# Optimization experiments

Measured on AMD Instinct MI355X. Metric: run time of the kernel, lower is better.

## Reference

```python
import jax, jax.numpy as jnp
import numpy as np

GAMMA = 0.99
CLIP_VALUE = 5.0
B, T = 4096, 2048


def setup_inputs() -> dict:
    key = jax.random.key(0)
    k1, k2, k3, k4 = jax.random.split(key, 4)
    return {
        "log_probs": jax.random.normal(k1, (B, T), dtype=jnp.float32),
        "logits": jax.random.normal(k2, (B, T, 1), dtype=jnp.float32),
        "weight": jax.random.uniform(k3, (B, T), dtype=jnp.float32),
        "baselines": jax.random.normal(k4, (B, T, 1), dtype=jnp.float32),
    }


def _discounted_cumulative(wr, gamma):
    # wr: [B, T]. cum[t] = sum_{s>=t} gamma^(s-t) * wr[s]
    # Reverse-time linear recurrence: c[t] = wr[t] + gamma * c[t+1]
    def step(c, x):
        c = x + gamma * c
        return c, c
    # scan over time in reverse; xs laid out time-major [T, B]
    _, cum_rev = jax.lax.scan(step, jnp.zeros(wr.shape[0], wr.dtype), wr[:, ::-1].T)
    return cum_rev[::-1].T  # back to [B, T]


def reference(log_probs, logits, weight, baselines):
    rewards = jax.nn.log_sigmoid(logits[..., 0])          # [B, T]
    cumulative_rewards = _discounted_cumulative(weight * rewards, GAMMA)  # [B, T]
    advantages = cumulative_rewards - baselines[..., 0]
    advantages = advantages - advantages.mean(axis=0)      # center over batch
    advantages = jnp.clip(advantages, -CLIP_VALUE, CLIP_VALUE)
    generator_objective = (advantages * log_probs).sum(axis=0)  # [T]
    return (generator_objective, cumulative_rewards)
```

## Files before the change

### kernel.cpp

```cpp
#include <hip/hip_runtime.h>
#include <math.h>

#define BDIM 4096
#define TDIM 2048
#define NBLK 512
#define RPB  8

constexpr double gpow(int e) {
    double r = 1.0;
    for (int i = 0; i < e; ++i) r *= 0.99;
    return r;
}

__device__ __forceinline__ float logsig_fast(float x) {
    float z = __expf(-fabsf(x));
    return fminf(x, 0.0f) - __logf(1.0f + z);
}

__device__ __forceinline__ float clip5(float x) {
    return fminf(fmaxf(x, -5.0f), 5.0f);
}

__global__ __launch_bounds__(512) void k1_scan(
    const float* __restrict__ logits,
    const float* __restrict__ weight,
    const float* __restrict__ baselines,
    float* __restrict__ cum_out,
    float* __restrict__ partial,
    float* __restrict__ colsum,
    float* __restrict__ obj)
{
    const int tid  = threadIdx.x;
    const int lane = tid & 63;
    const int wave = tid >> 6;
    const int t0   = tid * 4;

    if (blockIdx.x == 0) {
        *reinterpret_cast<float4*>(colsum + t0) = make_float4(0.f, 0.f, 0.f, 0.f);
    }
    if (blockIdx.x == 1) {
        *reinterpret_cast<float4*>(obj + t0) = make_float4(0.f, 0.f, 0.f, 0.f);
    }

    const float G    = 0.99f;
    const float G256 = (float)gpow(256);
    const float LOG2G = -0.014499569695115089f;
    const float gk[4] = {(float)gpow(4), (float)gpow(3), (float)gpow(2), (float)gpow(1)};
    const float fs[6] = {(float)gpow(4),  (float)gpow(8),  (float)gpow(16),
                         (float)gpow(32), (float)gpow(64), (float)gpow(128)};
    const float lane_pow = exp2f((float)((64 - lane) * 4) * LOG2G);

    __shared__ float wsum[2][8];

    float colacc[4];
#pragma unroll
    for (int k = 0; k < 4; ++k) colacc[k] = 0.0f;

    const int row0 = blockIdx.x * RPB;
    size_t base = (size_t)row0 * TDIM + t0;

    float4 x0 = *reinterpret_cast<const float4*>(logits + base);
    float4 w0 = *reinterpret_cast<const float4*>(weight + base);
    float4 b0 = *reinterpret_cast<const float4*>(baselines + base);

    for (int r = 0; r < RPB; ++r) {
        const size_t nbase = base + TDIM;
        const bool has_next = (r + 1 < RPB);

        float wr[4];
        wr[0] = w0.x * logsig_fast(x0.x); wr[1] = w0.y * logsig_fast(x0.y);
        wr[2] = w0.z * logsig_fast(x0.z); wr[3] = w0.w * logsig_fast(x0.w);

        float4 nx0, nw0, nb0;
        if (has_next) {
            nx0 = *reinterpret_cast<const float4*>(logits + nbase);
            nw0 = *reinterpret_cast<const float4*>(weight + nbase);
            nb0 = *reinterpret_cast<const float4*>(baselines + nbase);
        }

        float loc[4];
        loc[3] = wr[3];
#pragma unroll
        for (int k = 2; k >= 0; --k) loc[k] = fmaf(G, loc[k + 1], wr[k]);

        float v = loc[0];
#pragma unroll
        for (int s = 0; s < 6; ++s) {
            const int o = 1 << s;
            float up = __shfl_down(v, (unsigned)o, 64);
            if (lane + o < 64) v = fmaf(fs[s], up, v);
        }

        const int buf = r & 1;
        if (lane == 0) wsum[buf][wave] = v;
        __syncthreads();
        const float W1 = wsum[buf][1], W2 = wsum[buf][2], W3 = wsum[buf][3];
        const float W4 = wsum[buf][4], W5 = wsum[buf][5], W6 = wsum[buf][6];
        const float W7 = wsum[buf][7];
        const float C6 = W7;
        const float C5 = fmaf(G256, C6, W6);
        const float C4 = fmaf(G256, C5, W5);
        const float C3 = fmaf(G256, C4, W4);
        const float C2 = fmaf(G256, C3, W3);
        const float C1 = fmaf(G256, C2, W2);
        const float C0 = fmaf(G256, C1, W1);
        const float carry = (wave == 0) ? C0 : (wave == 1) ? C1 : (wave == 2) ? C2 :
                            (wave == 3) ? C3 : (wave == 4) ? C4 : (wave == 5) ? C5 :
                            (wave == 6) ? C6 : 0.0f;

        const float vfull = fmaf(lane_pow, carry, v);
        const float vn = __shfl_down(vfull, 1, 64);
        const float tail = (lane == 63) ? carry : vn;

        float c[4];
#pragma unroll
        for (int k = 0; k < 4; ++k) c[k] = fmaf(gk[k], tail, loc[k]);

        *reinterpret_cast<float4*>(cum_out + base) = make_float4(c[0], c[1], c[2], c[3]);

        colacc[0] += c[0] - b0.x; colacc[1] += c[1] - b0.y;
        colacc[2] += c[2] - b0.z; colacc[3] += c[3] - b0.w;

        base = nbase;
        if (has_next) {
            x0 = nx0; w0 = nw0; b0 = nb0;
        }
    }

    const size_t pbase = (size_t)blockIdx.x * TDIM + t0;
    *reinterpret_cast<float4*>(partial + pbase) =
        make_float4(colacc[0], colacc[1], colacc[2], colacc[3]);
}

__global__ __launch_bounds__(256) void k2_colsum(
    const float* __restrict__ partial, float* __restrict__ colsum)
{
    const int gid = blockIdx.x * 256 + threadIdx.x;
    const int col = gid & (TDIM - 1);
    const int slc = gid >> 11;
    const float* p = partial + (size_t)slc * 16 * TDIM + col;
    float s = 0.0f;
#pragma unroll
    for (int i = 0; i < 16; ++i) s += p[(size_t)i * TDIM];
    atomicAdd(colsum + col, s);
}

#define K3_ROWS 8
__global__ __launch_bounds__(256) void k3_part(
    const float* __restrict__ cum,
    const float* __restrict__ baselines,
    const float* __restrict__ lp,
    const float* __restrict__ colsum,
    float* __restrict__ objpart)
{
    const int c2 = (blockIdx.x * 256 + threadIdx.x) * 2;
    const int yb = blockIdx.y;
    const int r0 = yb * K3_ROWS;
    const float inv = 1.0f / (float)BDIM;
    float2 ms = *reinterpret_cast<const float2*>(colsum + c2);
    const float m0 = ms.x * inv, m1 = ms.y * inv;

    float a0 = 0.0f, a1 = 0.0f;
    size_t idx = (size_t)r0 * TDIM + c2;
#pragma unroll
    for (int r = 0; r < K3_ROWS; ++r, idx += TDIM) {
        float2 c = *reinterpret_cast<const float2*>(cum + idx);
        float2 b = *reinterpret_cast<const float2*>(baselines + idx);
        float2 l = *reinterpret_cast<const float2*>(lp + idx);
        a0 = fmaf(clip5(c.x - b.x - m0), l.x, a0);
        a1 = fmaf(clip5(c.y - b.y - m1), l.y, a1);
    }
    *reinterpret_cast<float2*>(objpart + (size_t)yb * TDIM + c2) = make_float2(a0, a1);
}

__global__ __launch_bounds__(256) void k4_objsum(
    const float* __restrict__ objpart, float* __restrict__ obj)
{
    const int gid = blockIdx.x * 256 + threadIdx.x;
    const int col = gid & (TDIM - 1);
    const int slc = gid >> 11;
    const float* p = objpart + (size_t)slc * 16 * TDIM + col;
    float s = 0.0f;
#pragma unroll
    for (int i = 0; i < 16; ++i) s += p[(size_t)i * TDIM];
    atomicAdd(obj + col, s);
}

extern "C" void kernel_launch(void* const* d_in, const int* in_sizes, int n_in,
                              void* d_out, int out_size, void* d_ws, size_t ws_size,
                              hipStream_t stream) {
    const float* log_probs = (const float*)d_in[0];
    const float* logits    = (const float*)d_in[1];
    const float* weight    = (const float*)d_in[2];
    const float* baselines = (const float*)d_in[3];

    float* out = (float*)d_out;
    float* obj = out;
    float* cum = out + TDIM;

    float* partial = (float*)d_ws;
    float* colsum  = partial + (size_t)NBLK * TDIM;

    k1_scan<<<NBLK, 512, 0, stream>>>(logits, weight, baselines, cum, partial, colsum, obj);
    k2_colsum<<<256, 256, 0, stream>>>(partial, colsum);
    k3_part<<<dim3(4, 512), 256, 0, stream>>>(cum, baselines, log_probs, colsum, partial);
    k4_objsum<<<256, 256, 0, stream>>>(partial, obj);
}
```

Baseline: 162.0 us.

## Scan each row with 1024 threads of two elements instead of 512 of four

The row-scan kernel now launches 1024 threads per block, each handling two time steps with float2 loads, instead of 512 threads handling four. The intra-wave shuffle scan and the 16-wave cross-wave carry chain are adjusted to the new powers of gamma. The aim is more threads in flight for latency hiding on the memory-bound pass. In exchange, loads are narrower, the serial carry chain across waves is longer, and the per-row block barrier now spans 16 waves.

Measured after the change: 163.1 us. About the same (+0.7%).

```diff
diff --git a/kernel.cpp b/kernel.cpp
--- a/kernel.cpp
+++ b/kernel.cpp
@@ -21,7 +21,7 @@
     return fminf(fmaxf(x, -5.0f), 5.0f);
 }
 
-__global__ __launch_bounds__(512) void k1_scan(
+__global__ __launch_bounds__(1024, 8) void k1_scan(
     const float* __restrict__ logits,
     const float* __restrict__ weight,
     const float* __restrict__ baselines,
@@ -33,55 +33,53 @@
     const int tid  = threadIdx.x;
     const int lane = tid & 63;
     const int wave = tid >> 6;
-    const int t0   = tid * 4;
+    const int t0   = tid * 2;
 
     if (blockIdx.x == 0) {
-        *reinterpret_cast<float4*>(colsum + t0) = make_float4(0.f, 0.f, 0.f, 0.f);
+        *reinterpret_cast<float2*>(colsum + t0) = make_float2(0.f, 0.f);
     }
     if (blockIdx.x == 1) {
-        *reinterpret_cast<float4*>(obj + t0) = make_float4(0.f, 0.f, 0.f, 0.f);
+        *reinterpret_cast<float2*>(obj + t0) = make_float2(0.f, 0.f);
     }
 
     const float G    = 0.99f;
-    const float G256 = (float)gpow(256);
+    const float G128 = (float)gpow(128);
     const float LOG2G = -0.014499569695115089f;
-    const float gk[4] = {(float)gpow(4), (float)gpow(3), (float)gpow(2), (float)gpow(1)};
-    const float fs[6] = {(float)gpow(4),  (float)gpow(8),  (float)gpow(16),
-                         (float)gpow(32), (float)gpow(64), (float)gpow(128)};
-    const float lane_pow = exp2f((float)((64 - lane) * 4) * LOG2G);
-
-    __shared__ float wsum[2][8];
-
-    float colacc[4];
-#pragma unroll
-    for (int k = 0; k < 4; ++k) colacc[k] = 0.0f;
+    const float gk[2] = {(float)gpow(2), (float)gpow(1)};
+    const float fs[6] = {(float)gpow(2),  (float)gpow(4),  (float)gpow(8),
+                         (float)gpow(16), (float)gpow(32), (float)gpow(64)};
+    const float lane_pow = exp2f((float)((64 - lane) * 2) * LOG2G);
+
+    __shared__ float wsum[2][16];
+
+    float colacc[2];
+    colacc[0] = 0.0f; colacc[1] = 0.0f;
 
     const int row0 = blockIdx.x * RPB;
     size_t base = (size_t)row0 * TDIM + t0;
 
-    float4 x0 = *reinterpret_cast<const float4*>(logits + base);
-    float4 w0 = *reinterpret_cast<const float4*>(weight + base);
-    float4 b0 = *reinterpret_cast<const float4*>(baselines + base);
+    float2 x0 = *reinterpret_cast<const float2*>(logits + base);
+    float2 w0 = *reinterpret_cast<const float2*>(weight + base);
+    float2 b0 = *reinterpret_cast<const float2*>(baselines + base);
 
     for (int r = 0; r < RPB; ++r) {
         const size_t nbase = base + TDIM;
         const bool has_next = (r + 1 < RPB);
 
-        float wr[4];
-        wr[0] = w0.x * logsig_fast(x0.x); wr[1] = w0.y * logsig_fast(x0.y);
-        wr[2] = w0.z * logsig_fast(x0.z); wr[3] = w0.w * logsig_fast(x0.w);
-
-        float4 nx0, nw0, nb0;
+        float wr[2];
+        wr[0] = w0.x * logsig_fast(x0.x);
+        wr[1] = w0.y * logsig_fast(x0.y);
+
+        float2 nx0, nw0, nb0;
         if (has_next) {
-            nx0 = *reinterpret_cast<const float4*>(logits + nbase);
-            nw0 = *reinterpret_cast<const float4*>(weight + nbase);
-            nb0 = *reinterpret_cast<const float4*>(baselines + nbase);
+            nx0 = *reinterpret_cast<const float2*>(logits + nbase);
+            nw0 = *reinterpret_cast<const float2*>(weight + nbase);
+            nb0 = *reinterpret_cast<const float2*>(baselines + nbase);
         }
 
-        float loc[4];
-        loc[3] = wr[3];
-#pragma unroll
-        for (int k = 2; k >= 0; --k) loc[k] = fmaf(G, loc[k + 1], wr[k]);
+        float loc[2];
+        loc[1] = wr[1];
+        loc[0] = fmaf(G, wr[1], wr[0]);
 
         float v = loc[0];
 #pragma unroll
@@ -94,32 +92,45 @@
         const int buf = r & 1;
         if (lane == 0) wsum[buf][wave] = v;
         __syncthreads();
-        const float W1 = wsum[buf][1], W2 = wsum[buf][2], W3 = wsum[buf][3];
-        const float W4 = wsum[buf][4], W5 = wsum[buf][5], W6 = wsum[buf][6];
-        const float W7 = wsum[buf][7];
-        const float C6 = W7;
-        const float C5 = fmaf(G256, C6, W6);
-        const float C4 = fmaf(G256, C5, W5);
-        const float C3 = fmaf(G256, C4, W4);
-        const float C2 = fmaf(G256, C3, W3);
-        const float C1 = fmaf(G256, C2, W2);
-        const float C0 = fmaf(G256, C1, W1);
-        const float carry = (wave == 0) ? C0 : (wave == 1) ? C1 : (wave == 2) ? C2 :
-                            (wave == 3) ? C3 : (wave == 4) ? C4 : (wave == 5) ? C5 :
-                            (wave == 6) ? C6 : 0.0f;
+        const float W1  = wsum[buf][1],  W2  = wsum[buf][2],  W3  = wsum[buf][3];
+        const float W4  = wsum[buf][4],  W5  = wsum[buf][5],  W6  = wsum[buf][6];
+        const float W7  = wsum[buf][7],  W8  = wsum[buf][8],  W9  = wsum[buf][9];
+        const float W10 = wsum[buf][10], W11 = wsum[buf][11], W12 = wsum[buf][12];
+        const float W13 = wsum[buf][13], W14 = wsum[buf][14], W15 = wsum[buf][15];
+        const float C14 = W15;
+        const float C13 = fmaf(G128, C14, W14);
+        const float C12 = fmaf(G128, C13, W13);
+        const float C11 = fmaf(G128, C12, W12);
+        const float C10 = fmaf(G128, C11, W11);
+        const float C9  = fmaf(G128, C10, W10);
+        const float C8  = fmaf(G128, C9,  W9);
+        const float C7  = fmaf(G128, C8,  W8);
+        const float C6  = fmaf(G128, C7,  W7);
+        const float C5  = fmaf(G128, C6,  W6);
+        const float C4  = fmaf(G128, C5,  W5);
+        const float C3  = fmaf(G128, C4,  W4);
+        const float C2  = fmaf(G128, C3,  W3);
+        const float C1  = fmaf(G128, C2,  W2);
+        const float C0  = fmaf(G128, C1,  W1);
+        const float carry =
+            (wave == 0)  ? C0  : (wave == 1)  ? C1  : (wave == 2)  ? C2  :
+            (wave == 3)  ? C3  : (wave == 4)  ? C4  : (wave == 5)  ? C5  :
+            (wave == 6)  ? C6  : (wave == 7)  ? C7  : (wave == 8)  ? C8  :
+            (wave == 9)  ? C9  : (wave == 10) ? C10 : (wave == 11) ? C11 :
+            (wave == 12) ? C12 : (wave == 13) ? C13 : (wave == 14) ? C14 : 0.0f;
 
         const float vfull = fmaf(lane_pow, carry, v);
         const float vn = __shfl_down(vfull, 1, 64);
         const float tail = (lane == 63) ? carry : vn;
 
-        float c[4];
-#pragma unroll
-        for (int k = 0; k < 4; ++k) c[k] = fmaf(gk[k], tail, loc[k]);
-
-        *reinterpret_cast<float4*>(cum_out + base) = make_float4(c[0], c[1], c[2], c[3]);
-
-        colacc[0] += c[0] - b0.x; colacc[1] += c[1] - b0.y;
-        colacc[2] += c[2] - b0.z; colacc[3] += c[3] - b0.w;
+        float c[2];
+        c[0] = fmaf(gk[0], tail, loc[0]);
+        c[1] = fmaf(gk[1], tail, loc[1]);
+
+        *reinterpret_cast<float2*>(cum_out + base) = make_float2(c[0], c[1]);
+
+        colacc[0] += c[0] - b0.x;
+        colacc[1] += c[1] - b0.y;
 
         base = nbase;
         if (has_next) {
@@ -128,8 +139,7 @@
     }
 
     const size_t pbase = (size_t)blockIdx.x * TDIM + t0;
-    *reinterpret_cast<float4*>(partial + pbase) =
-        make_float4(colacc[0], colacc[1], colacc[2], colacc[3]);
+    *reinterpret_cast<float2*>(partial + pbase) = make_float2(colacc[0], colacc[1]);
 }
 
 __global__ __launch_bounds__(256) void k2_colsum(
@@ -201,7 +211,7 @@
     float* partial = (float*)d_ws;
     float* colsum  = partial + (size_t)NBLK * TDIM;
 
-    k1_scan<<<NBLK, 512, 0, stream>>>(logits, weight, baselines, cum, partial, colsum, obj);
+    k1_scan<<<NBLK, 1024, 0, stream>>>(logits, weight, baselines, cum, partial, colsum, obj);
     k2_colsum<<<256, 256, 0, stream>>>(partial, colsum);
     k3_part<<<dim3(4, 512), 256, 0, stream>>>(cum, baselines, log_probs, colsum, partial);
     k4_objsum<<<256, 256, 0, stream>>>(partial, obj);
```

## Assign one wave per row with 32 contiguous elements per lane in scan kernel

Applied to the files above, without the earlier changes.

The scan kernel changes from a whole block cooperating on one row at a time (with a block-wide barrier per row) to one wave per row, where each lane holds 32 contiguous timesteps. Each lane does a serial local scan, then a single wave shuffle scan completes the row. This removes the per-row __syncthreads and cross-wave carry. Column partial sums now go through shared-memory atomics in a transposed layout, which adds LDS atomic traffic and higher register pressure (96 loaded floats per lane).

Result: slower. 209.8 us (+29.5%).

```diff
diff --git a/kernel.cpp b/kernel.cpp
--- a/kernel.cpp
+++ b/kernel.cpp
@@ -4,7 +4,6 @@
 #define BDIM 4096
 #define TDIM 2048
 #define NBLK 512
-#define RPB  8
 
 constexpr double gpow(int e) {
     double r = 1.0;
@@ -21,7 +20,7 @@
     return fminf(fmaxf(x, -5.0f), 5.0f);
 }
 
-__global__ __launch_bounds__(512) void k1_scan(
+__global__ __launch_bounds__(512, 4) void k1_scan(
     const float* __restrict__ logits,
     const float* __restrict__ weight,
     const float* __restrict__ baselines,
@@ -33,103 +32,96 @@
     const int tid  = threadIdx.x;
     const int lane = tid & 63;
     const int wave = tid >> 6;
-    const int t0   = tid * 4;
 
     if (blockIdx.x == 0) {
-        *reinterpret_cast<float4*>(colsum + t0) = make_float4(0.f, 0.f, 0.f, 0.f);
+        *reinterpret_cast<float4*>(colsum + tid * 4) = make_float4(0.f, 0.f, 0.f, 0.f);
     }
     if (blockIdx.x == 1) {
-        *reinterpret_cast<float4*>(obj + t0) = make_float4(0.f, 0.f, 0.f, 0.f);
-    }
-
-    const float G    = 0.99f;
-    const float G256 = (float)gpow(256);
-    const float LOG2G = -0.014499569695115089f;
-    const float gk[4] = {(float)gpow(4), (float)gpow(3), (float)gpow(2), (float)gpow(1)};
-    const float fs[6] = {(float)gpow(4),  (float)gpow(8),  (float)gpow(16),
-                         (float)gpow(32), (float)gpow(64), (float)gpow(128)};
-    const float lane_pow = exp2f((float)((64 - lane) * 4) * LOG2G);
-
-    __shared__ float wsum[2][8];
-
-    float colacc[4];
-#pragma unroll
-    for (int k = 0; k < 4; ++k) colacc[k] = 0.0f;
-
-    const int row0 = blockIdx.x * RPB;
-    size_t base = (size_t)row0 * TDIM + t0;
-
-    float4 x0 = *reinterpret_cast<const float4*>(logits + base);
-    float4 w0 = *reinterpret_cast<const float4*>(weight + base);
-    float4 b0 = *reinterpret_cast<const float4*>(baselines + base);
-
-    for (int r = 0; r < RPB; ++r) {
-        const size_t nbase = base + TDIM;
-        const bool has_next = (r + 1 < RPB);
-
-        float wr[4];
-        wr[0] = w0.x * logsig_fast(x0.x); wr[1] = w0.y * logsig_fast(x0.y);
-        wr[2] = w0.z * logsig_fast(x0.z); wr[3] = w0.w * logsig_fast(x0.w);
-
-        float4 nx0, nw0, nb0;
-        if (has_next) {
-            nx0 = *reinterpret_cast<const float4*>(logits + nbase);
-            nw0 = *reinterpret_cast<const float4*>(weight + nbase);
-            nb0 = *reinterpret_cast<const float4*>(baselines + nbase);
-        }
-
-        float loc[4];
-        loc[3] = wr[3];
-#pragma unroll
-        for (int k = 2; k >= 0; --k) loc[k] = fmaf(G, loc[k + 1], wr[k]);
-
-        float v = loc[0];
-#pragma unroll
-        for (int s = 0; s < 6; ++s) {
-            const int o = 1 << s;
-            float up = __shfl_down(v, (unsigned)o, 64);
-            if (lane + o < 64) v = fmaf(fs[s], up, v);
-        }
-
-        const int buf = r & 1;
-        if (lane == 0) wsum[buf][wave] = v;
-        __syncthreads();
-        const float W1 = wsum[buf][1], W2 = wsum[buf][2], W3 = wsum[buf][3];
-        const float W4 = wsum[buf][4], W5 = wsum[buf][5], W6 = wsum[buf][6];
-        const float W7 = wsum[buf][7];
-        const float C6 = W7;
-        const float C5 = fmaf(G256, C6, W6);
-        const float C4 = fmaf(G256, C5, W5);
-        const float C3 = fmaf(G256, C4, W4);
-        const float C2 = fmaf(G256, C3, W3);
-        const float C1 = fmaf(G256, C2, W2);
-        const float C0 = fmaf(G256, C1, W1);
-        const float carry = (wave == 0) ? C0 : (wave == 1) ? C1 : (wave == 2) ? C2 :
-                            (wave == 3) ? C3 : (wave == 4) ? C4 : (wave == 5) ? C5 :
-                            (wave == 6) ? C6 : 0.0f;
-
-        const float vfull = fmaf(lane_pow, carry, v);
-        const float vn = __shfl_down(vfull, 1, 64);
-        const float tail = (lane == 63) ? carry : vn;
-
-        float c[4];
-#pragma unroll
-        for (int k = 0; k < 4; ++k) c[k] = fmaf(gk[k], tail, loc[k]);
-
-        *reinterpret_cast<float4*>(cum_out + base) = make_float4(c[0], c[1], c[2], c[3]);
-
-        colacc[0] += c[0] - b0.x; colacc[1] += c[1] - b0.y;
-        colacc[2] += c[2] - b0.z; colacc[3] += c[3] - b0.w;
-
-        base = nbase;
-        if (has_next) {
-            x0 = nx0; w0 = nw0; b0 = nb0;
-        }
-    }
-
-    const size_t pbase = (size_t)blockIdx.x * TDIM + t0;
-    *reinterpret_cast<float4*>(partial + pbase) =
-        make_float4(colacc[0], colacc[1], colacc[2], colacc[3]);
+        *reinterpret_cast<float4*>(obj + tid * 4) = make_float4(0.f, 0.f, 0.f, 0.f);
+    }
+
+    const float G = 0.99f;
+    const float fsw[6] = {(float)gpow(32),  (float)gpow(64),  (float)gpow(128),
+                          (float)gpow(256), (float)gpow(512), (float)gpow(1024)};
+    const float gt[32] = {
+        (float)gpow(32), (float)gpow(31), (float)gpow(30), (float)gpow(29),
+        (float)gpow(28), (float)gpow(27), (float)gpow(26), (float)gpow(25),
+        (float)gpow(24), (float)gpow(23), (float)gpow(22), (float)gpow(21),
+        (float)gpow(20), (float)gpow(19), (float)gpow(18), (float)gpow(17),
+        (float)gpow(16), (float)gpow(15), (float)gpow(14), (float)gpow(13),
+        (float)gpow(12), (float)gpow(11), (float)gpow(10), (float)gpow(9),
+        (float)gpow(8),  (float)gpow(7),  (float)gpow(6),  (float)gpow(5),
+        (float)gpow(4),  (float)gpow(3),  (float)gpow(2),  (float)gpow(1)};
+
+    __shared__ __align__(16) float cacc[TDIM];
+
+    *reinterpret_cast<float4*>(&cacc[tid * 4]) = make_float4(0.f, 0.f, 0.f, 0.f);
+    __syncthreads();
+
+    const int row = blockIdx.x * 8 + wave;
+    const size_t rbase = (size_t)row * TDIM + (size_t)lane * 32;
+
+    float4 xq[8], wq[8], bq[8];
+#pragma unroll
+    for (int j = 0; j < 8; ++j) xq[j] = *reinterpret_cast<const float4*>(logits + rbase + j * 4);
+#pragma unroll
+    for (int j = 0; j < 8; ++j) wq[j] = *reinterpret_cast<const float4*>(weight + rbase + j * 4);
+#pragma unroll
+    for (int j = 0; j < 8; ++j) bq[j] = *reinterpret_cast<const float4*>(baselines + rbase + j * 4);
+
+    float wr[32];
+#pragma unroll
+    for (int j = 0; j < 8; ++j) {
+        wr[j * 4 + 0] = wq[j].x * logsig_fast(xq[j].x);
+        wr[j * 4 + 1] = wq[j].y * logsig_fast(xq[j].y);
+        wr[j * 4 + 2] = wq[j].z * logsig_fast(xq[j].z);
+        wr[j * 4 + 3] = wq[j].w * logsig_fast(xq[j].w);
+    }
+#pragma unroll
+    for (int k = 30; k >= 0; --k) wr[k] = fmaf(G, wr[k + 1], wr[k]);
+
+    float v = wr[0];
+#pragma unroll
+    for (int s = 0; s < 6; ++s) {
+        const int o = 1 << s;
+        float up = __shfl_down(v, (unsigned)o, 64);
+        if (lane + o < 64) v = fmaf(fsw[s], up, v);
+    }
+    const float vn = __shfl_down(v, 1, 64);
+    const float tail = (lane == 63) ? 0.0f : vn;
+
+    float c[32];
+#pragma unroll
+    for (int k = 0; k < 32; ++k) c[k] = fmaf(gt[k], tail, wr[k]);
+
+#pragma unroll
+    for (int j = 0; j < 8; ++j) {
+        *reinterpret_cast<float4*>(cum_out + rbase + j * 4) =
+            make_float4(c[j * 4 + 0], c[j * 4 + 1], c[j * 4 + 2], c[j * 4 + 3]);
+    }
+
+    float bv[32];
+#pragma unroll
+    for (int j = 0; j < 8; ++j) {
+        bv[j * 4 + 0] = bq[j].x; bv[j * 4 + 1] = bq[j].y;
+        bv[j * 4 + 2] = bq[j].z; bv[j * 4 + 3] = bq[j].w;
+    }
+
+#pragma unroll
+    for (int k = 0; k < 32; ++k) {
+        atomicAdd(&cacc[k * 64 + lane], c[k] - bv[k]);
+    }
+    __syncthreads();
+
+    {
+        const int col0 = tid * 4;
+        float4 p;
+        p.x = cacc[((col0 + 0) & 31) * 64 + ((col0 + 0) >> 5)];
+        p.y = cacc[((col0 + 1) & 31) * 64 + ((col0 + 1) >> 5)];
+        p.z = cacc[((col0 + 2) & 31) * 64 + ((col0 + 2) >> 5)];
+        p.w = cacc[((col0 + 3) & 31) * 64 + ((col0 + 3) >> 5)];
+        *reinterpret_cast<float4*>(partial + (size_t)blockIdx.x * TDIM + col0) = p;
+    }
 }
 
 __global__ __launch_bounds__(256) void k2_colsum(
```
